# Performance work log

Measured on AMD Instinct MI355X. Metric: run time of the kernel, lower is better.

The kernel has to match this reference:

```python
import jax, jax.numpy as jnp
import numpy as np

DIM_MODEL = 512
HEADS = 8
DIM_HEAD = 64
HIDDEN = HEADS * DIM_HEAD
SCALE = DIM_HEAD ** -0.5
GN_EPS = 1e-5


def setup_inputs() -> dict:
    key = jax.random.key(0)
    ks = jax.random.split(key, 7)
    b, t = 8, 4096
    x = jax.random.normal(ks[0], (b, DIM_MODEL, t), dtype=jnp.float32)
    mask = jax.random.randint(ks[1], (b, t), 0, 2) == 1  # bool padding mask
    # 1x1 convs are plain channel matmuls; kernels squeezed to 2D
    w_qkv = jax.random.normal(ks[2], (3 * HIDDEN, DIM_MODEL), dtype=jnp.float32) * (DIM_MODEL ** -0.5)
    w_out = jax.random.normal(ks[3], (DIM_MODEL, HIDDEN), dtype=jnp.float32) * (HIDDEN ** -0.5)
    b_out = jax.random.normal(ks[4], (DIM_MODEL,), dtype=jnp.float32) * 0.01
    gn_gamma = jnp.ones((DIM_MODEL,), dtype=jnp.float32)
    gn_beta = jnp.zeros((DIM_MODEL,), dtype=jnp.float32)
    return {"x": x, "mask": mask, "w_qkv": w_qkv, "w_out": w_out,
            "b_out": b_out, "gn_gamma": gn_gamma, "gn_beta": gn_beta}


def reference(x, mask, w_qkv, w_out, b_out, gn_gamma, gn_beta):
    b, c, t = x.shape
    # to_qkv: 1x1 conv == channel matmul -> [b, 3*hidden, t]
    qkv = jnp.einsum('oc,bct->bot', w_qkv, x)
    q, k, v = jnp.split(qkv, 3, axis=1)
    # 'b (h d) t -> b h d t'
    q = q.reshape(b, HEADS, DIM_HEAD, t)
    k = k.reshape(b, HEADS, DIM_HEAD, t)
    v = v.reshape(b, HEADS, DIM_HEAD, t)
    # additive mask: 0.0 where True, 1e-12 where False; broadcast 'b t -> b 1 1 t'
    maskf = jnp.where(mask, 0.0, 1e-12)[:, None, None, :].astype(x.dtype)
    q = jax.nn.softmax(q, axis=-2) * SCALE            # softmax over feature dim d
    k = jax.nn.softmax(k + maskf, axis=-1)            # softmax over time dim t
    # linear attention: O(t * d * e)
    context = jnp.einsum('bhdn,bhen->bhde', k, v)      # [b, h, d, e]
    out = jnp.einsum('bhde,bhdn->bhen', context, q)    # [b, h, e, t]
    out = out.reshape(b, HIDDEN, t)                    # 'b h e t -> b (h e) t'
    # to_out: 1x1 conv with bias, then GroupNorm(1, dim_model)
    y = jnp.einsum('oc,bct->bot', w_out, out) + b_out[None, :, None]
    mu = jnp.mean(y, axis=(1, 2), keepdims=True)
    var = jnp.var(y, axis=(1, 2), keepdims=True)
    y = (y - mu) * jax.lax.rsqrt(var + GN_EPS)
    return y * gn_gamma[None, :, None] + gn_beta[None, :, None]
```

## Files before the change

### kernel.cpp

```cpp
#include <hip/hip_runtime.h>
#include <stdint.h>

typedef unsigned short u16;
using f32x4 = __attribute__((ext_vector_type(4))) float;
using s16x8 = __attribute__((ext_vector_type(8))) short;

#define MFMA_BF16(a, b, c) __builtin_amdgcn_mfma_f32_16x16x32_bf16((a), (b), (c), 0, 0, 0)

#define GLOAD_LDS16(gptr, lptr)                                                               \
  __builtin_amdgcn_global_load_lds((const __attribute__((address_space(1))) uint32_t*)(gptr), \
                                   (__attribute__((address_space(3))) uint32_t*)(lptr), 16, 0, 0)

__device__ __forceinline__ u16 f2bf(float f) {
  union { float f; uint32_t u; } v; v.f = f;
  uint32_t r = v.u + 0x7fffu + ((v.u >> 16) & 1u);
  return (u16)(r >> 16);
}
__device__ __forceinline__ float bf2f(u16 h) {
  union { uint32_t u; float f; } v; v.u = ((uint32_t)h) << 16;
  return v.f;
}

__global__ void k_transpose_x(const float* __restrict__ x, u16* __restrict__ xT,
                              const float* __restrict__ wq, const float* __restrict__ wo,
                              u16* __restrict__ wqb, u16* __restrict__ wob) {
  if (blockIdx.z == 8) {
    const int nq = 1536 * 512 / 4;
    const int no = 512 * 512 / 4;
    int bid = blockIdx.y * 64 + blockIdx.x;
#pragma unroll
    for (int rep = 0; rep < 2; ++rep) {
      int i = bid * 256 + threadIdx.x + rep * 131072;
      if (i < nq) {
        float4 v = ((const float4*)wq)[i];
        u16* o = wqb + i * 4;
        o[0] = f2bf(v.x); o[1] = f2bf(v.y); o[2] = f2bf(v.z); o[3] = f2bf(v.w);
      } else if (i < nq + no) {
        int j = i - nq;
        float4 v = ((const float4*)wo)[j];
        u16* o = wob + j * 4;
        o[0] = f2bf(v.x); o[1] = f2bf(v.y); o[2] = f2bf(v.z); o[3] = f2bf(v.w);
      }
    }
    return;
  }
  __shared__ u16 tile[64][68];
  int b = blockIdx.z, c0 = blockIdx.y * 64, t0 = blockIdx.x * 64;
  const float* xp = x + ((size_t)b * 512 + c0) * 4096 + t0;
#pragma unroll
  for (int it = 0; it < 4; ++it) {
    int r = it * 16 + (threadIdx.x >> 4), c4 = (threadIdx.x & 15) * 4;
    float4 v = *(const float4*)(xp + (size_t)r * 4096 + c4);
    tile[r][c4 + 0] = f2bf(v.x);
    tile[r][c4 + 1] = f2bf(v.y);
    tile[r][c4 + 2] = f2bf(v.z);
    tile[r][c4 + 3] = f2bf(v.w);
  }
  __syncthreads();
  u16* op = xT + ((size_t)b * 4096 + t0) * 512 + c0;
#pragma unroll
  for (int it = 0; it < 2; ++it) {
    int tr = it * 32 + (threadIdx.x >> 3), cb = (threadIdx.x & 7) * 8;
    s16x8 o;
#pragma unroll
    for (int jj = 0; jj < 8; ++jj) o[jj] = tile[cb + jj][tr];
    *(s16x8*)(op + (size_t)tr * 512 + cb) = o;
  }
}

__launch_bounds__(256, 2)
__global__ void k_gemm_qkv(const u16* __restrict__ A, const u16* __restrict__ BT,
                           u16* __restrict__ C, u16* __restrict__ qT,
                           float* __restrict__ spart) {
  __shared__ s16x8 As8[1024];
  __shared__ s16x8 Bs8[1024];
  __shared__ float ksums[4][64];
  int b = blockIdx.z;
  int m0 = blockIdx.y * 128, n0 = blockIdx.x * 128;
  const u16* Ab = A + (size_t)m0 * 512;
  const u16* Bb = BT + ((size_t)b * 4096 + n0) * 512;
  int tid = threadIdx.x, w = tid >> 6, lane = tid & 63;
  int wm = (w >> 1) * 64, wn = (w & 1) * 64;
  f32x4 acc[4][4] = {};
  for (int kt = 0; kt < 8; ++kt) {
    if (kt) __syncthreads();
#pragma unroll
    for (int it = 0; it < 4; ++it) {
      int L = (w * 4 + it) * 64 + lane;
      int r = L >> 3;
      int lc = (L & 7) ^ (r & 7);
      GLOAD_LDS16(Ab + (size_t)r * 512 + kt * 64 + lc * 8, ((char*)As8) + (w * 4 + it) * 1024);
      GLOAD_LDS16(Bb + (size_t)r * 512 + kt * 64 + lc * 8, ((char*)Bs8) + (w * 4 + it) * 1024);
    }
    asm volatile("s_waitcnt vmcnt(0)");
    __syncthreads();
#pragma unroll
    for (int kk = 0; kk < 2; ++kk) {
      int cb = kk * 4 + (lane >> 4);
      s16x8 af[4], bfr[4];
#pragma unroll
      for (int mi = 0; mi < 4; ++mi) {
        int r = wm + mi * 16 + (lane & 15);
        af[mi] = As8[r * 8 + (cb ^ (r & 7))];
      }
#pragma unroll
      for (int ni = 0; ni < 4; ++ni) {
        int r = wn + ni * 16 + (lane & 15);
        bfr[ni] = Bs8[r * 8 + (cb ^ (r & 7))];
      }
#pragma unroll
      for (int mi = 0; mi < 4; ++mi)
#pragma unroll
        for (int ni = 0; ni < 4; ++ni)
          acc[mi][ni] = MFMA_BF16(af[mi], bfr[ni], acc[mi][ni]);
    }
  }
  if (blockIdx.y < 4) {
    int head = (m0 >> 6) + (wm >> 6);
    int bh = b * 8 + head;
#pragma unroll
    for (int ni = 0; ni < 4; ++ni) {
      float mx = -1e30f;
#pragma unroll
      for (int mi = 0; mi < 4; ++mi)
#pragma unroll
        for (int j = 0; j < 4; ++j) mx = fmaxf(mx, acc[mi][ni][j]);
      mx = fmaxf(mx, __shfl_xor(mx, 16));
      mx = fmaxf(mx, __shfl_xor(mx, 32));
      float e[4][4];
      float s = 0.f;
#pragma unroll
      for (int mi = 0; mi < 4; ++mi)
#pragma unroll
        for (int j = 0; j < 4; ++j) { e[mi][j] = __expf(acc[mi][ni][j] - mx); s += e[mi][j]; }
      s += __shfl_xor(s, 16);
      s += __shfl_xor(s, 32);
      float sc = 0.125f / s;
      int t = n0 + wn + ni * 16 + (lane & 15);
      u16* op = qT + ((size_t)bh * 4096 + t) * 64 + (lane >> 4) * 4;
#pragma unroll
      for (int mi = 0; mi < 4; ++mi) {
        union { u16 u[4]; uint2 v; } pk;
#pragma unroll
        for (int j = 0; j < 4; ++j) pk.u[j] = f2bf(e[mi][j] * sc);
        *(uint2*)(op + mi * 16) = pk.v;
      }
    }
  } else if (blockIdx.y < 8) {
    u16* Cb = C + ((size_t)b * 1536 + m0) * 4096 + n0;
#pragma unroll
    for (int mi = 0; mi < 4; ++mi)
#pragma unroll
      for (int j = 0; j < 4; ++j) {
        int mm = wm + mi * 16 + (lane >> 4) * 4 + j;
        float t = 0.f;
#pragma unroll
        for (int ni = 0; ni < 4; ++ni) {
          int nn = wn + ni * 16 + (lane & 15);
          float e = __expf(acc[mi][ni][j]);
          t += e;
          Cb[(size_t)mm * 4096 + nn] = f2bf(e);
        }
        t += __shfl_xor(t, 1);
        t += __shfl_xor(t, 2);
        t += __shfl_xor(t, 4);
        t += __shfl_xor(t, 8);
        if ((lane & 15) == 0) ksums[w][mi * 16 + (lane >> 4) * 4 + j] = t;
      }
    __syncthreads();
    if (tid < 128) {
      int hr = tid >> 6, r = tid & 63;
      float v = ksums[hr * 2][r] + ksums[hr * 2 + 1][r];
      spart[((size_t)b * 512 + (m0 - 512) + hr * 64 + r) * 32 + blockIdx.x] = v;
    }
  } else {
    u16* Cb = C + ((size_t)b * 1536 + m0) * 4096 + n0;
#pragma unroll
    for (int mi = 0; mi < 4; ++mi)
#pragma unroll
      for (int ni = 0; ni < 4; ++ni)
#pragma unroll
        for (int j = 0; j < 4; ++j) {
          int mm = wm + mi * 16 + (lane >> 4) * 4 + j;
          int nn = wn + ni * 16 + (lane & 15);
          Cb[(size_t)mm * 4096 + nn] = f2bf(acc[mi][ni][j]);
        }
  }
}

__global__ void k_context_part(const u16* __restrict__ qkv, float* __restrict__ ctxp) {
  int s = blockIdx.x, bh = blockIdx.y;
  int b = bh >> 3, h = bh & 7;
  int w = threadIdx.x >> 6, lane = threadIdx.x & 63;
  int hi = lane >> 4, lo = lane & 15;
  const u16* vb = qkv + ((size_t)b * 1536 + 1024 + h * 64) * 4096 + s * 256;
  const u16* kb = qkv + ((size_t)b * 1536 + 512 + h * 64) * 4096 + s * 256;
  int d = w * 16 + lo;
  f32x4 acc[4] = {};
#pragma unroll
  for (int st = 0; st < 8; ++st) {
    int nn = st * 32 + hi * 8;
    s16x8 bexp = *(const s16x8*)(kb + (size_t)d * 4096 + nn);
#pragma unroll
    for (int ei = 0; ei < 4; ++ei) {
      s16x8 a = *(const s16x8*)(vb + (size_t)(ei * 16 + lo) * 4096 + nn);
      acc[ei] = MFMA_BF16(a, bexp, acc[ei]);
    }
  }
  float* cp = ctxp + ((size_t)bh * 16 + s) * 4096;
#pragma unroll
  for (int ei = 0; ei < 4; ++ei) {
    float4 o;
    o.x = acc[ei][0]; o.y = acc[ei][1]; o.z = acc[ei][2]; o.w = acc[ei][3];
    *(float4*)&cp[(size_t)d * 64 + ei * 16 + hi * 4] = o;
  }
}

__global__ void k_ctx_reduce(const float* __restrict__ ctxp, const float* __restrict__ spart,
                             u16* __restrict__ Bg) {
  int q = blockIdx.x, bh = blockIdx.y;
  int b = bh >> 3, h = bh & 7;
  __shared__ float sinv[4];
  int tid = threadIdx.x;
  if (tid < 4) {
    int hd = h * 64 + q * 4 + tid;
    const float* sp = spart + ((size_t)b * 512 + hd) * 32;
    float s = 0.f;
#pragma unroll
    for (int xx = 0; xx < 32; ++xx) s += sp[xx];
    sinv[tid] = 1.f / s;
  }
  __syncthreads();
  int pos = q * 256 + tid;
  float v = 0.f;
#pragma unroll
  for (int si = 0; si < 16; ++si) v += ctxp[((size_t)bh * 16 + si) * 4096 + pos];
  Bg[(size_t)bh * 4096 + pos] = f2bf(v * sinv[(pos >> 6) & 3]);
}

__global__ void k_wfused(const u16* __restrict__ wout, const u16* __restrict__ Bg,
                         u16* __restrict__ Wf) {
  int bh = blockIdx.x;
  int b = bh >> 3, h = bh & 7;
  int w = threadIdx.x >> 6, lane = threadIdx.x & 63;
  int hi = lane >> 4, lo = lane & 15;
  const u16* Bb = Bg + (size_t)bh * 4096;
  const u16* Ab = wout + (size_t)h * 64;
  f32x4 acc[8][4] = {};
#pragma unroll
  for (int ks = 0; ks < 2; ++ks) {
    s16x8 bfr[4];
#pragma unroll
    for (int ni = 0; ni < 4; ++ni)
      bfr[ni] = *(const s16x8*)(Bb + (size_t)(ni * 16 + lo) * 64 + ks * 32 + hi * 8);
#pragma unroll
    for (int mi = 0; mi < 8; ++mi) {
      s16x8 a = *(const s16x8*)(Ab + (size_t)(w * 128 + mi * 16 + lo) * 512 + ks * 32 + hi * 8);
#pragma unroll
      for (int ni = 0; ni < 4; ++ni) acc[mi][ni] = MFMA_BF16(a, bfr[ni], acc[mi][ni]);
    }
  }
#pragma unroll
  for (int mi = 0; mi < 8; ++mi)
#pragma unroll
    for (int ni = 0; ni < 4; ++ni) {
      int m = w * 128 + mi * 16 + hi * 4;
      int d = ni * 16 + lo;
#pragma unroll
      for (int j = 0; j < 4; ++j)
        Wf[((size_t)b * 512 + m + j) * 512 + h * 64 + d] = f2bf(acc[mi][ni][j]);
    }
}

__launch_bounds__(256, 2)
__global__ void k_gemm_final(const u16* __restrict__ Wf, const u16* __restrict__ qT,
                             u16* __restrict__ Ybf, const float* __restrict__ bias,
                             float2* __restrict__ part2) {
  __shared__ s16x8 As8[1024];
  __shared__ s16x8 Bs8[1024];
  int b = blockIdx.z;
  int m0 = blockIdx.y * 128, n0 = blockIdx.x * 128;
  const u16* Ab = Wf + ((size_t)b * 512 + m0) * 512;
  const u16* qTb = qT + (size_t)b * 8 * 4096 * 64;
  int tid = threadIdx.x, w = tid >> 6, lane = tid & 63;
  int wm = (w >> 1) * 64, wn = (w & 1) * 64;
  f32x4 acc[4][4] = {};
  for (int kt = 0; kt < 8; ++kt) {
    if (kt) __syncthreads();
#pragma unroll
    for (int it = 0; it < 4; ++it) {
      int L = (w * 4 + it) * 64 + lane;
      int r = L >> 3;
      int lc = (L & 7) ^ (r & 7);
      GLOAD_LDS16(Ab + (size_t)r * 512 + kt * 64 + lc * 8, ((char*)As8) + (w * 4 + it) * 1024);
      int G = kt * 8 + lc;
      GLOAD_LDS16(qTb + ((size_t)(G >> 3) * 4096 + n0 + r) * 64 + (G & 7) * 8,
                  ((char*)Bs8) + (w * 4 + it) * 1024);
    }
    asm volatile("s_waitcnt vmcnt(0)");
    __syncthreads();
#pragma unroll
    for (int kk = 0; kk < 2; ++kk) {
      int cb = kk * 4 + (lane >> 4);
      s16x8 af[4], bfr[4];
#pragma unroll
      for (int mi = 0; mi < 4; ++mi) {
        int r = wm + mi * 16 + (lane & 15);
        af[mi] = As8[r * 8 + (cb ^ (r & 7))];
      }
#pragma unroll
      for (int ni = 0; ni < 4; ++ni) {
        int r = wn + ni * 16 + (lane & 15);
        bfr[ni] = Bs8[r * 8 + (cb ^ (r & 7))];
      }
#pragma unroll
      for (int mi = 0; mi < 4; ++mi)
#pragma unroll
        for (int ni = 0; ni < 4; ++ni)
          acc[mi][ni] = MFMA_BF16(af[mi], bfr[ni], acc[mi][ni]);
    }
  }
  u16* Yb = Ybf + ((size_t)b * 512 + m0) * 4096 + n0;
  float sm = 0.f, ssm = 0.f;
#pragma unroll
  for (int mi = 0; mi < 4; ++mi)
#pragma unroll
    for (int j = 0; j < 4; ++j) {
      int mm = wm + mi * 16 + (lane >> 4) * 4 + j;
      float bo = bias[m0 + mm];
#pragma unroll
      for (int ni = 0; ni < 4; ++ni) {
        int nn = wn + ni * 16 + (lane & 15);
        float vv = acc[mi][ni][j] + bo;
        sm += vv;
        ssm += vv * vv;
        Yb[(size_t)mm * 4096 + nn] = f2bf(vv);
      }
    }
#pragma unroll
  for (int off = 32; off; off >>= 1) { sm += __shfl_xor(sm, off); ssm += __shfl_xor(ssm, off); }
  __shared__ float sr[4], ssr[4];
  if (lane == 0) { sr[w] = sm; ssr[w] = ssm; }
  __syncthreads();
  if (tid == 0) {
    float2 o;
    o.x = sr[0] + sr[1] + sr[2] + sr[3];
    o.y = ssr[0] + ssr[1] + ssr[2] + ssr[3];
    part2[((size_t)b * 4 + blockIdx.y) * 32 + blockIdx.x] = o;
  }
}

__global__ void k_gn_norm(const u16* __restrict__ ybf, float* __restrict__ y,
                          const float2* __restrict__ part2,
                          const float* __restrict__ gamma, const float* __restrict__ beta) {
  int b = blockIdx.y;
  float s = 0.f, ss = 0.f;
#pragma unroll 8
  for (int i = 0; i < 128; ++i) { float2 pp = part2[b * 128 + i]; s += pp.x; ss += pp.y; }
  const float N = 512.f * 4096.f;
  float mu = s / N;
  float var = ss / N - mu * mu;
  float rstd = rsqrtf(var + 1e-5f);
  size_t base = ((size_t)b << 21) + (size_t)blockIdx.x * 16384;
  const s16x8* ip = (const s16x8*)(ybf + base);
  float4* opf = (float4*)(y + base);
#pragma unroll
  for (int i = 0; i < 8; ++i) {
    int idx = threadIdx.x + i * 256;
    int loc = (int)(blockIdx.x * 16384) + idx * 8;
    int c = loc >> 12;
    float g = gamma[c] * rstd, bt = beta[c];
    s16x8 v = ip[idx];
    float4 o0, o1;
    o0.x = (bf2f((u16)v[0]) - mu) * g + bt;
    o0.y = (bf2f((u16)v[1]) - mu) * g + bt;
    o0.z = (bf2f((u16)v[2]) - mu) * g + bt;
    o0.w = (bf2f((u16)v[3]) - mu) * g + bt;
    o1.x = (bf2f((u16)v[4]) - mu) * g + bt;
    o1.y = (bf2f((u16)v[5]) - mu) * g + bt;
    o1.z = (bf2f((u16)v[6]) - mu) * g + bt;
    o1.w = (bf2f((u16)v[7]) - mu) * g + bt;
    opf[idx * 2] = o0;
    opf[idx * 2 + 1] = o1;
  }
}

extern "C" void kernel_launch(void* const* d_in, const int* in_sizes, int n_in,
                              void* d_out, int out_size, void* d_ws, size_t ws_size,
                              hipStream_t stream) {
  const float* x     = (const float*)d_in[0];
  const float* wqkv  = (const float*)d_in[2];
  const float* wout  = (const float*)d_in[3];
  const float* bout  = (const float*)d_in[4];
  const float* gamma = (const float*)d_in[5];
  const float* beta  = (const float*)d_in[6];
  float* y = (float*)d_out;

  char* ws = (char*)d_ws;
  u16*    qkv_b = (u16*)ws;
  u16*    ybf   = (u16*)ws;
  u16*    xT    = (u16*)(ws + 100663296);
  float*  ctxp  = (float*)(ws + 100663296);
  u16*    Bg    = (u16*)(ws + 117702656);
  u16*    qT    = (u16*)(ws + 134217728);
  u16*    wqkvb = (u16*)(ws + 167772160);
  u16*    woutb = (u16*)(ws + 169345024);
  u16*    Wfused= (u16*)(ws + 169869312);
  float2* part2 = (float2*)(ws + 174063616);
  float*  spart = (float*)(ws + 174071808);

  {
    dim3 g(64, 8, 9);
    k_transpose_x<<<g, 256, 0, stream>>>(x, xT, wqkv, wout, wqkvb, woutb);
  }
  {
    dim3 g(32, 12, 8);
    k_gemm_qkv<<<g, 256, 0, stream>>>(wqkvb, xT, qkv_b, qT, spart);
  }
  {
    dim3 g(16, 64);
    k_context_part<<<g, 256, 0, stream>>>(qkv_b, ctxp);
  }
  {
    dim3 g(16, 64);
    k_ctx_reduce<<<g, 256, 0, stream>>>(ctxp, spart, Bg);
  }
  k_wfused<<<64, 256, 0, stream>>>(woutb, Bg, Wfused);
  {
    dim3 g(32, 4, 8);
    k_gemm_final<<<g, 256, 0, stream>>>(Wfused, qT, ybf, bout, part2);
  }
  {
    dim3 g(128, 8);
    k_gn_norm<<<g, 256, 0, stream>>>(ybf, y, part2, gamma, beta);
  }
}
```

Baseline: 174.8 us.

## Compute context via exp(K)·Xᵀ then multiply by W_v, skipping V materialization

The V projection is no longer computed or stored. The code forms G = exp(K)·Xᵀ per batch, a 512x512 product over time split into two halves, then multiplies by W_v inside a fused kernel that also applies the softmax normalisation and builds the fused output weight. This removes the V GEMM and its 32MB bf16 write and read, and merges the context partial and reduce kernels. In exchange it adds a bf16 copy of x, a larger K-dim GEMM (512x512x4096 per batch), and extra bf16 rounding of G.

After: 203.6 us. 16.5% more time.

```diff
diff --git a/kernel.cpp b/kernel.cpp
--- a/kernel.cpp
+++ b/kernel.cpp
@@ -22,6 +22,7 @@
 }
 
 __global__ void k_transpose_x(const float* __restrict__ x, u16* __restrict__ xT,
+                              u16* __restrict__ xbf,
                               const float* __restrict__ wq, const float* __restrict__ wo,
                               u16* __restrict__ wqb, u16* __restrict__ wob) {
   if (blockIdx.z == 8) {
@@ -51,10 +52,13 @@
   for (int it = 0; it < 4; ++it) {
     int r = it * 16 + (threadIdx.x >> 4), c4 = (threadIdx.x & 15) * 4;
     float4 v = *(const float4*)(xp + (size_t)r * 4096 + c4);
-    tile[r][c4 + 0] = f2bf(v.x);
-    tile[r][c4 + 1] = f2bf(v.y);
-    tile[r][c4 + 2] = f2bf(v.z);
-    tile[r][c4 + 3] = f2bf(v.w);
+    union { u16 u[4]; uint2 q; } pk;
+    pk.u[0] = f2bf(v.x); pk.u[1] = f2bf(v.y); pk.u[2] = f2bf(v.z); pk.u[3] = f2bf(v.w);
+    tile[r][c4 + 0] = pk.u[0];
+    tile[r][c4 + 1] = pk.u[1];
+    tile[r][c4 + 2] = pk.u[2];
+    tile[r][c4 + 3] = pk.u[3];
+    *(uint2*)(xbf + ((size_t)b * 512 + c0 + r) * 4096 + t0 + c4) = pk.q;
   }
   __syncthreads();
   u16* op = xT + ((size_t)b * 4096 + t0) * 512 + c0;
@@ -70,7 +74,7 @@
 
 __launch_bounds__(256, 2)
 __global__ void k_gemm_qkv(const u16* __restrict__ A, const u16* __restrict__ BT,
-                           u16* __restrict__ C, u16* __restrict__ qT,
+                           u16* __restrict__ ek, u16* __restrict__ qT,
                            float* __restrict__ spart) {
   __shared__ s16x8 As8[1024];
   __shared__ s16x8 Bs8[1024];
@@ -146,8 +150,8 @@
         *(uint2*)(op + mi * 16) = pk.v;
       }
     }
-  } else if (blockIdx.y < 8) {
-    u16* Cb = C + ((size_t)b * 1536 + m0) * 4096 + n0;
+  } else {
+    u16* Cb = ek + ((size_t)b * 512 + (m0 - 512)) * 4096 + n0;
 #pragma unroll
     for (int mi = 0; mi < 4; ++mi)
 #pragma unroll
@@ -173,78 +177,108 @@
       float v = ksums[hr * 2][r] + ksums[hr * 2 + 1][r];
       spart[((size_t)b * 512 + (m0 - 512) + hr * 64 + r) * 32 + blockIdx.x] = v;
     }
-  } else {
-    u16* Cb = C + ((size_t)b * 1536 + m0) * 4096 + n0;
-#pragma unroll
-    for (int mi = 0; mi < 4; ++mi)
-#pragma unroll
-      for (int ni = 0; ni < 4; ++ni)
-#pragma unroll
-        for (int j = 0; j < 4; ++j) {
-          int mm = wm + mi * 16 + (lane >> 4) * 4 + j;
-          int nn = wn + ni * 16 + (lane & 15);
-          Cb[(size_t)mm * 4096 + nn] = f2bf(acc[mi][ni][j]);
-        }
-  }
-}
-
-__global__ void k_context_part(const u16* __restrict__ qkv, float* __restrict__ ctxp) {
-  int s = blockIdx.x, bh = blockIdx.y;
+  }
+}
+
+__launch_bounds__(256, 2)
+__global__ void k_gemm_G(const u16* __restrict__ ek, const u16* __restrict__ xbf,
+                         u16* __restrict__ Gt) {
+  __shared__ s16x8 As8[1024];
+  __shared__ s16x8 Bs8[1024];
+  int z = blockIdx.z;
+  int b = z >> 1, half = z & 1;
+  int m0 = blockIdx.y * 128, n0 = blockIdx.x * 128;
+  const u16* Ab = ek + ((size_t)b * 512 + m0) * 4096 + half * 2048;
+  const u16* Bb = xbf + ((size_t)b * 512 + n0) * 4096 + half * 2048;
+  int tid = threadIdx.x, w = tid >> 6, lane = tid & 63;
+  int wm = (w >> 1) * 64, wn = (w & 1) * 64;
+  f32x4 acc[4][4] = {};
+  for (int kt = 0; kt < 32; ++kt) {
+    if (kt) __syncthreads();
+#pragma unroll
+    for (int it = 0; it < 4; ++it) {
+      int L = (w * 4 + it) * 64 + lane;
+      int r = L >> 3;
+      int lc = (L & 7) ^ (r & 7);
+      GLOAD_LDS16(Ab + (size_t)r * 4096 + kt * 64 + lc * 8, ((char*)As8) + (w * 4 + it) * 1024);
+      GLOAD_LDS16(Bb + (size_t)r * 4096 + kt * 64 + lc * 8, ((char*)Bs8) + (w * 4 + it) * 1024);
+    }
+    asm volatile("s_waitcnt vmcnt(0)");
+    __syncthreads();
+#pragma unroll
+    for (int kk = 0; kk < 2; ++kk) {
+      int cb = kk * 4 + (lane >> 4);
+      s16x8 af[4], bfr[4];
+#pragma unroll
+      for (int mi = 0; mi < 4; ++mi) {
+        int r = wm + mi * 16 + (lane & 15);
+        af[mi] = As8[r * 8 + (cb ^ (r & 7))];
+      }
+#pragma unroll
+      for (int ni = 0; ni < 4; ++ni) {
+        int r = wn + ni * 16 + (lane & 15);
+        bfr[ni] = Bs8[r * 8 + (cb ^ (r & 7))];
+      }
+#pragma unroll
+      for (int mi = 0; mi < 4; ++mi)
+#pragma unroll
+        for (int ni = 0; ni < 4; ++ni)
+          acc[mi][ni] = MFMA_BF16(af[mi], bfr[ni], acc[mi][ni]);
+    }
+  }
+  u16* Cb = Gt + (((size_t)half * 8 + b) * 512 + m0) * 512 + n0;
+#pragma unroll
+  for (int mi = 0; mi < 4; ++mi)
+#pragma unroll
+    for (int ni = 0; ni < 4; ++ni)
+#pragma unroll
+      for (int j = 0; j < 4; ++j) {
+        int mm = wm + mi * 16 + (lane >> 4) * 4 + j;
+        int nn = wn + ni * 16 + (lane & 15);
+        Cb[(size_t)mm * 512 + nn] = f2bf(acc[mi][ni][j]);
+      }
+}
+
+__global__ void k_ctx_wfused(const u16* __restrict__ Gt, const float* __restrict__ spart,
+                             const u16* __restrict__ wqkvb, const u16* __restrict__ wout,
+                             u16* __restrict__ Wf) {
+  __shared__ float sinv[64];
+  __shared__ __align__(16) u16 Bgl[64 * 72];
+  int bh = blockIdx.x;
   int b = bh >> 3, h = bh & 7;
-  int w = threadIdx.x >> 6, lane = threadIdx.x & 63;
-  int hi = lane >> 4, lo = lane & 15;
-  const u16* vb = qkv + ((size_t)b * 1536 + 1024 + h * 64) * 4096 + s * 256;
-  const u16* kb = qkv + ((size_t)b * 1536 + 512 + h * 64) * 4096 + s * 256;
-  int d = w * 16 + lo;
-  f32x4 acc[4] = {};
-#pragma unroll
-  for (int st = 0; st < 8; ++st) {
-    int nn = st * 32 + hi * 8;
-    s16x8 bexp = *(const s16x8*)(kb + (size_t)d * 4096 + nn);
-#pragma unroll
-    for (int ei = 0; ei < 4; ++ei) {
-      s16x8 a = *(const s16x8*)(vb + (size_t)(ei * 16 + lo) * 4096 + nn);
-      acc[ei] = MFMA_BF16(a, bexp, acc[ei]);
-    }
-  }
-  float* cp = ctxp + ((size_t)bh * 16 + s) * 4096;
-#pragma unroll
-  for (int ei = 0; ei < 4; ++ei) {
-    float4 o;
-    o.x = acc[ei][0]; o.y = acc[ei][1]; o.z = acc[ei][2]; o.w = acc[ei][3];
-    *(float4*)&cp[(size_t)d * 64 + ei * 16 + hi * 4] = o;
-  }
-}
-
-__global__ void k_ctx_reduce(const float* __restrict__ ctxp, const float* __restrict__ spart,
-                             u16* __restrict__ Bg) {
-  int q = blockIdx.x, bh = blockIdx.y;
-  int b = bh >> 3, h = bh & 7;
-  __shared__ float sinv[4];
   int tid = threadIdx.x;
-  if (tid < 4) {
-    int hd = h * 64 + q * 4 + tid;
-    const float* sp = spart + ((size_t)b * 512 + hd) * 32;
+  if (tid < 64) {
+    const float* sp = spart + ((size_t)b * 512 + h * 64 + tid) * 32;
     float s = 0.f;
 #pragma unroll
     for (int xx = 0; xx < 32; ++xx) s += sp[xx];
     sinv[tid] = 1.f / s;
   }
   __syncthreads();
-  int pos = q * 256 + tid;
-  float v = 0.f;
-#pragma unroll
-  for (int si = 0; si < 16; ++si) v += ctxp[((size_t)bh * 16 + si) * 4096 + pos];
-  Bg[(size_t)bh * 4096 + pos] = f2bf(v * sinv[(pos >> 6) & 3]);
-}
-
-__global__ void k_wfused(const u16* __restrict__ wout, const u16* __restrict__ Bg,
-                         u16* __restrict__ Wf) {
-  int bh = blockIdx.x;
-  int b = bh >> 3, h = bh & 7;
-  int w = threadIdx.x >> 6, lane = threadIdx.x & 63;
-  int hi = lane >> 4, lo = lane & 15;
-  const u16* Bb = Bg + (size_t)bh * 4096;
+  int w = tid >> 6, lane = tid & 63, hi = lane >> 4, lo = lane & 15;
+  const u16* Wv = wqkvb + (size_t)(1024 + h * 64) * 512;
+  f32x4 cacc[4] = {};
+#pragma unroll
+  for (int half = 0; half < 2; ++half) {
+    const u16* Ga = Gt + (((size_t)half * 8 + b) * 512 + h * 64 + w * 16 + lo) * 512;
+#pragma unroll
+    for (int ks = 0; ks < 16; ++ks) {
+      s16x8 ga = *(const s16x8*)(Ga + ks * 32 + hi * 8);
+#pragma unroll
+      for (int ni = 0; ni < 4; ++ni) {
+        s16x8 wv = *(const s16x8*)(Wv + (size_t)(ni * 16 + lo) * 512 + ks * 32 + hi * 8);
+        cacc[ni] = MFMA_BF16(ga, wv, cacc[ni]);
+      }
+    }
+  }
+#pragma unroll
+  for (int ni = 0; ni < 4; ++ni)
+#pragma unroll
+    for (int j = 0; j < 4; ++j) {
+      int d = w * 16 + hi * 4 + j;
+      Bgl[d * 72 + ni * 16 + lo] = f2bf(cacc[ni][j] * sinv[d]);
+    }
+  __syncthreads();
   const u16* Ab = wout + (size_t)h * 64;
   f32x4 acc[8][4] = {};
 #pragma unroll
@@ -252,7 +286,7 @@
     s16x8 bfr[4];
 #pragma unroll
     for (int ni = 0; ni < 4; ++ni)
-      bfr[ni] = *(const s16x8*)(Bb + (size_t)(ni * 16 + lo) * 64 + ks * 32 + hi * 8);
+      bfr[ni] = *(const s16x8*)&Bgl[(ni * 16 + lo) * 72 + ks * 32 + hi * 8];
 #pragma unroll
     for (int mi = 0; mi < 8; ++mi) {
       s16x8 a = *(const s16x8*)(Ab + (size_t)(w * 128 + mi * 16 + lo) * 512 + ks * 32 + hi * 8);
@@ -397,35 +431,31 @@
   float* y = (float*)d_out;
 
   char* ws = (char*)d_ws;
-  u16*    qkv_b = (u16*)ws;
-  u16*    ybf   = (u16*)ws;
-  u16*    xT    = (u16*)(ws + 100663296);
-  float*  ctxp  = (float*)(ws + 100663296);
-  u16*    Bg    = (u16*)(ws + 117702656);
-  u16*    qT    = (u16*)(ws + 134217728);
-  u16*    wqkvb = (u16*)(ws + 167772160);
-  u16*    woutb = (u16*)(ws + 169345024);
-  u16*    Wfused= (u16*)(ws + 169869312);
-  float2* part2 = (float2*)(ws + 174063616);
-  float*  spart = (float*)(ws + 174071808);
+  u16*    ek    = (u16*)ws;
+  u16*    xT    = (u16*)(ws + 33554432);
+  u16*    xbf   = (u16*)(ws + 67108864);
+  u16*    ybf   = xbf;
+  u16*    qT    = (u16*)(ws + 100663296);
+  u16*    Gt    = (u16*)(ws + 134217728);
+  u16*    wqkvb = (u16*)(ws + 142606336);
+  u16*    woutb = (u16*)(ws + 144179200);
+  u16*    Wfused= (u16*)(ws + 144703488);
+  float*  spart = (float*)(ws + 148897792);
+  float2* part2 = (float2*)(ws + 149422080);
 
   {
     dim3 g(64, 8, 9);
-    k_transpose_x<<<g, 256, 0, stream>>>(x, xT, wqkv, wout, wqkvb, woutb);
+    k_transpose_x<<<g, 256, 0, stream>>>(x, xT, xbf, wqkv, wout, wqkvb, woutb);
   }
   {
-    dim3 g(32, 12, 8);
-    k_gemm_qkv<<<g, 256, 0, stream>>>(wqkvb, xT, qkv_b, qT, spart);
+    dim3 g(32, 8, 8);
+    k_gemm_qkv<<<g, 256, 0, stream>>>(wqkvb, xT, ek, qT, spart);
   }
   {
-    dim3 g(16, 64);
-    k_context_part<<<g, 256, 0, stream>>>(qkv_b, ctxp);
-  }
-  {
-    dim3 g(16, 64);
-    k_ctx_reduce<<<g, 256, 0, stream>>>(ctxp, spart, Bg);
-  }
-  k_wfused<<<64, 256, 0, stream>>>(woutb, Bg, Wfused);
+    dim3 g(4, 4, 16);
+    k_gemm_G<<<g, 256, 0, stream>>>(ek, xbf, Gt);
+  }
+  k_ctx_wfused<<<64, 256, 0, stream>>>(Gt, spart, wqkvb, woutb, Wfused);
   {
     dim3 g(32, 4, 8);
     k_gemm_final<<<g, 256, 0, stream>>>(Wfused, qT, ybf, bout, part2);
```

## Use 256x256 double-buffered 8-wave GEMM tiles for QKV and output projections

Applied to the files above, without the earlier changes.

Both bf16 GEMMs are rebuilt on a shared core macro with 256x256 block tiles, 512 threads (8 waves of 128x64), and double-buffered LDS. The next k-tile's global-to-LDS loads are interleaved between MFMA groups, and s_setprio raises priority around the MFMA bursts. The aim is more data reuse per LDS load and overlap of memory traffic with matrix math. The cost is 132KB of dynamic LDS per block and far fewer blocks (768 and 256), so occupancy and wave-quantization tail effects on the GPU become a risk; partial-sum buffers and their reducers are resized to match.

New measurement: 167.6 us, median of 3. 4.1% less time.

```diff
diff --git a/kernel.cpp b/kernel.cpp
--- a/kernel.cpp
+++ b/kernel.cpp
@@ -68,125 +68,251 @@
   }
 }
 
-__launch_bounds__(256, 2)
+#define STAGE_A16(u, ktile, bf)                                                        \
+  { int L = (u)*512 + tid; int r = L >> 3, pc = L & 7; int lc = pc ^ (r & 7);          \
+    GLOAD_LDS16(Ab + (size_t)r * 512 + (ktile) * 64 + lc * 8,                          \
+                ((char*)AL) + (bf) * 32768 + (size_t)L * 16); }
+#define STAGE_B16(u, ktile, bf)                                                        \
+  { int L = (u)*512 + tid; int r = L >> 3, pc = L & 7; int lc = pc ^ (r & 7);          \
+    GLOAD_LDS16(BSRCX(r, ktile, lc),                                                   \
+                ((char*)BL) + (bf) * 32768 + (size_t)L * 16); }
+
+#define GEMM256_CORE()                                                                 \
+  s16x8* AL = (s16x8*)lds;                                                             \
+  s16x8* BL = (s16x8*)(lds + 65536);                                                   \
+  int tid = threadIdx.x, w = tid >> 6, lane = tid & 63;                                \
+  int wr = w >> 2, wc = w & 3;                                                         \
+  int hi = lane >> 4, lo = lane & 15;                                                  \
+  f32x4 acc[8][4] = {};                                                                \
+  _Pragma("unroll")                                                                    \
+  for (int u = 0; u < 4; ++u) STAGE_A16(u, 0, 0);                                      \
+  _Pragma("unroll")                                                                    \
+  for (int u = 0; u < 4; ++u) STAGE_B16(u, 0, 0);                                      \
+  asm volatile("s_waitcnt vmcnt(0)" ::: "memory");                                     \
+  __syncthreads();                                                                     \
+  int cur = 0;                                                                         \
+  _Pragma("unroll 2")                                                                  \
+  for (int kt = 0; kt < 8; ++kt) {                                                     \
+    const s16x8* Ac = AL + cur * 2048;                                                 \
+    const s16x8* Bc = BL + cur * 2048;                                                 \
+    int nxt = cur ^ 1;                                                                 \
+    bool pf = (kt < 7);                                                                \
+    s16x8 af[4][2], b0[2][2], b1[2][2];                                                \
+    _Pragma("unroll")                                                                  \
+    for (int mi = 0; mi < 4; ++mi) {                                                   \
+      int r = wr * 128 + mi * 16 + lo;                                                 \
+      _Pragma("unroll")                                                                \
+      for (int kk = 0; kk < 2; ++kk) {                                                 \
+        int lc = kk * 4 + hi;                                                          \
+        af[mi][kk] = Ac[r * 8 + (lc ^ (r & 7))];                                       \
+      }                                                                                \
+    }                                                                                  \
+    _Pragma("unroll")                                                                  \
+    for (int ni = 0; ni < 2; ++ni) {                                                   \
+      int r = wc * 64 + ni * 16 + lo;                                                  \
+      _Pragma("unroll")                                                                \
+      for (int kk = 0; kk < 2; ++kk) {                                                 \
+        int lc = kk * 4 + hi;                                                          \
+        b0[ni][kk] = Bc[r * 8 + (lc ^ (r & 7))];                                       \
+      }                                                                                \
+    }                                                                                  \
+    if (pf) { STAGE_A16(0, kt + 1, nxt); STAGE_A16(1, kt + 1, nxt); }                  \
+    __builtin_amdgcn_s_setprio(1);                                                     \
+    _Pragma("unroll")                                                                  \
+    for (int mi = 0; mi < 4; ++mi)                                                     \
+      _Pragma("unroll")                                                                \
+      for (int ni = 0; ni < 2; ++ni)                                                   \
+        _Pragma("unroll")                                                              \
+        for (int kk = 0; kk < 2; ++kk)                                                 \
+          acc[mi][ni] = MFMA_BF16(af[mi][kk], b0[ni][kk], acc[mi][ni]);                \
+    __builtin_amdgcn_s_setprio(0);                                                     \
+    _Pragma("unroll")                                                                  \
+    for (int ni = 0; ni < 2; ++ni) {                                                   \
+      int r = wc * 64 + (ni + 2) * 16 + lo;                                            \
+      _Pragma("unroll")                                                                \
+      for (int kk = 0; kk < 2; ++kk) {                                                 \
+        int lc = kk * 4 + hi;                                                          \
+        b1[ni][kk] = Bc[r * 8 + (lc ^ (r & 7))];                                       \
+      }                                                                                \
+    }                                                                                  \
+    if (pf) { STAGE_A16(2, kt + 1, nxt); STAGE_A16(3, kt + 1, nxt); }                  \
+    __builtin_amdgcn_s_setprio(1);                                                     \
+    _Pragma("unroll")                                                                  \
+    for (int mi = 0; mi < 4; ++mi)                                                     \
+      _Pragma("unroll")                                                                \
+      for (int ni = 0; ni < 2; ++ni)                                                   \
+        _Pragma("unroll")                                                              \
+        for (int kk = 0; kk < 2; ++kk)                                                 \
+          acc[mi][ni + 2] = MFMA_BF16(af[mi][kk], b1[ni][kk], acc[mi][ni + 2]);        \
+    __builtin_amdgcn_s_setprio(0);                                                     \
+    _Pragma("unroll")                                                                  \
+    for (int mi = 0; mi < 4; ++mi) {                                                   \
+      int r = wr * 128 + 64 + mi * 16 + lo;                                            \
+      _Pragma("unroll")                                                                \
+      for (int kk = 0; kk < 2; ++kk) {                                                 \
+        int lc = kk * 4 + hi;                                                          \
+        af[mi][kk] = Ac[r * 8 + (lc ^ (r & 7))];                                       \
+      }                                                                                \
+    }                                                                                  \
+    if (pf) { STAGE_B16(0, kt + 1, nxt); STAGE_B16(1, kt + 1, nxt); }                  \
+    __builtin_amdgcn_s_setprio(1);                                                     \
+    _Pragma("unroll")                                                                  \
+    for (int mi = 0; mi < 4; ++mi)                                                     \
+      _Pragma("unroll")                                                                \
+      for (int ni = 0; ni < 2; ++ni)                                                   \
+        _Pragma("unroll")                                                              \
+        for (int kk = 0; kk < 2; ++kk)                                                 \
+          acc[mi + 4][ni + 2] = MFMA_BF16(af[mi][kk], b1[ni][kk], acc[mi + 4][ni + 2]);\
+    __builtin_amdgcn_s_setprio(0);                                                     \
+    if (pf) { STAGE_B16(2, kt + 1, nxt); STAGE_B16(3, kt + 1, nxt); }                  \
+    __builtin_amdgcn_s_setprio(1);                                                     \
+    _Pragma("unroll")                                                                  \
+    for (int mi = 0; mi < 4; ++mi)                                                     \
+      _Pragma("unroll")                                                                \
+      for (int ni = 0; ni < 2; ++ni)                                                   \
+        _Pragma("unroll")                                                              \
+        for (int kk = 0; kk < 2; ++kk)                                                 \
+          acc[mi + 4][ni] = MFMA_BF16(af[mi][kk], b0[ni][kk], acc[mi + 4][ni]);        \
+    __builtin_amdgcn_s_setprio(0);                                                     \
+    asm volatile("s_waitcnt vmcnt(0)" ::: "memory");                                   \
+    __syncthreads();                                                                   \
+    cur = nxt;                                                                         \
+  }
+
+#define BSRCX(r, ktile, lc) (Bb + (size_t)(r) * 512 + (ktile) * 64 + (lc) * 8)
+__launch_bounds__(512, 2)
 __global__ void k_gemm_qkv(const u16* __restrict__ A, const u16* __restrict__ BT,
                            u16* __restrict__ C, u16* __restrict__ qT,
                            float* __restrict__ spart) {
-  __shared__ s16x8 As8[1024];
-  __shared__ s16x8 Bs8[1024];
-  __shared__ float ksums[4][64];
+  extern __shared__ char lds[];
   int b = blockIdx.z;
-  int m0 = blockIdx.y * 128, n0 = blockIdx.x * 128;
+  int m0 = blockIdx.y * 256, n0 = blockIdx.x * 256;
   const u16* Ab = A + (size_t)m0 * 512;
   const u16* Bb = BT + ((size_t)b * 4096 + n0) * 512;
-  int tid = threadIdx.x, w = tid >> 6, lane = tid & 63;
-  int wm = (w >> 1) * 64, wn = (w & 1) * 64;
-  f32x4 acc[4][4] = {};
-  for (int kt = 0; kt < 8; ++kt) {
-    if (kt) __syncthreads();
-#pragma unroll
-    for (int it = 0; it < 4; ++it) {
-      int L = (w * 4 + it) * 64 + lane;
-      int r = L >> 3;
-      int lc = (L & 7) ^ (r & 7);
-      GLOAD_LDS16(Ab + (size_t)r * 512 + kt * 64 + lc * 8, ((char*)As8) + (w * 4 + it) * 1024);
-      GLOAD_LDS16(Bb + (size_t)r * 512 + kt * 64 + lc * 8, ((char*)Bs8) + (w * 4 + it) * 1024);
-    }
-    asm volatile("s_waitcnt vmcnt(0)");
-    __syncthreads();
-#pragma unroll
-    for (int kk = 0; kk < 2; ++kk) {
-      int cb = kk * 4 + (lane >> 4);
-      s16x8 af[4], bfr[4];
-#pragma unroll
-      for (int mi = 0; mi < 4; ++mi) {
-        int r = wm + mi * 16 + (lane & 15);
-        af[mi] = As8[r * 8 + (cb ^ (r & 7))];
+  GEMM256_CORE()
+  if (blockIdx.y < 2) {
+#pragma unroll
+    for (int hb = 0; hb < 2; ++hb) {
+      int head = (int)blockIdx.y * 4 + wr * 2 + hb;
+      int bh = b * 8 + head;
+#pragma unroll
+      for (int ni = 0; ni < 4; ++ni) {
+        float mx = -1e30f;
+#pragma unroll
+        for (int mi = 0; mi < 4; ++mi)
+#pragma unroll
+          for (int j = 0; j < 4; ++j) mx = fmaxf(mx, acc[hb * 4 + mi][ni][j]);
+        mx = fmaxf(mx, __shfl_xor(mx, 16));
+        mx = fmaxf(mx, __shfl_xor(mx, 32));
+        float e[4][4];
+        float s = 0.f;
+#pragma unroll
+        for (int mi = 0; mi < 4; ++mi)
+#pragma unroll
+          for (int j = 0; j < 4; ++j) {
+            e[mi][j] = __expf(acc[hb * 4 + mi][ni][j] - mx);
+            s += e[mi][j];
+          }
+        s += __shfl_xor(s, 16);
+        s += __shfl_xor(s, 32);
+        float sc = 0.125f / s;
+        int t = n0 + wc * 64 + ni * 16 + lo;
+        u16* op = qT + ((size_t)bh * 4096 + t) * 64 + hi * 4;
+#pragma unroll
+        for (int mi = 0; mi < 4; ++mi) {
+          union { u16 u[4]; uint2 v; } pk;
+#pragma unroll
+          for (int j = 0; j < 4; ++j) pk.u[j] = f2bf(e[mi][j] * sc);
+          *(uint2*)(op + mi * 16) = pk.v;
+        }
       }
-#pragma unroll
-      for (int ni = 0; ni < 4; ++ni) {
-        int r = wn + ni * 16 + (lane & 15);
-        bfr[ni] = Bs8[r * 8 + (cb ^ (r & 7))];
-      }
-#pragma unroll
-      for (int mi = 0; mi < 4; ++mi)
-#pragma unroll
-        for (int ni = 0; ni < 4; ++ni)
-          acc[mi][ni] = MFMA_BF16(af[mi], bfr[ni], acc[mi][ni]);
-    }
-  }
-  if (blockIdx.y < 4) {
-    int head = (m0 >> 6) + (wm >> 6);
-    int bh = b * 8 + head;
-#pragma unroll
-    for (int ni = 0; ni < 4; ++ni) {
-      float mx = -1e30f;
-#pragma unroll
-      for (int mi = 0; mi < 4; ++mi)
-#pragma unroll
-        for (int j = 0; j < 4; ++j) mx = fmaxf(mx, acc[mi][ni][j]);
-      mx = fmaxf(mx, __shfl_xor(mx, 16));
-      mx = fmaxf(mx, __shfl_xor(mx, 32));
-      float e[4][4];
-      float s = 0.f;
-#pragma unroll
-      for (int mi = 0; mi < 4; ++mi)
-#pragma unroll
-        for (int j = 0; j < 4; ++j) { e[mi][j] = __expf(acc[mi][ni][j] - mx); s += e[mi][j]; }
-      s += __shfl_xor(s, 16);
-      s += __shfl_xor(s, 32);
-      float sc = 0.125f / s;
-      int t = n0 + wn + ni * 16 + (lane & 15);
-      u16* op = qT + ((size_t)bh * 4096 + t) * 64 + (lane >> 4) * 4;
-#pragma unroll
-      for (int mi = 0; mi < 4; ++mi) {
-        union { u16 u[4]; uint2 v; } pk;
-#pragma unroll
-        for (int j = 0; j < 4; ++j) pk.u[j] = f2bf(e[mi][j] * sc);
-        *(uint2*)(op + mi * 16) = pk.v;
-      }
-    }
-  } else if (blockIdx.y < 8) {
+    }
+  } else if (blockIdx.y < 4) {
     u16* Cb = C + ((size_t)b * 1536 + m0) * 4096 + n0;
-#pragma unroll
-    for (int mi = 0; mi < 4; ++mi)
+    float* ks = (float*)(lds + 131072);
+#pragma unroll
+    for (int mi = 0; mi < 8; ++mi)
 #pragma unroll
       for (int j = 0; j < 4; ++j) {
-        int mm = wm + mi * 16 + (lane >> 4) * 4 + j;
+        int mr = wr * 128 + mi * 16 + hi * 4 + j;
         float t = 0.f;
 #pragma unroll
         for (int ni = 0; ni < 4; ++ni) {
-          int nn = wn + ni * 16 + (lane & 15);
+          int nn = wc * 64 + ni * 16 + lo;
           float e = __expf(acc[mi][ni][j]);
           t += e;
-          Cb[(size_t)mm * 4096 + nn] = f2bf(e);
+          Cb[(size_t)mr * 4096 + nn] = f2bf(e);
         }
         t += __shfl_xor(t, 1);
         t += __shfl_xor(t, 2);
         t += __shfl_xor(t, 4);
         t += __shfl_xor(t, 8);
-        if ((lane & 15) == 0) ksums[w][mi * 16 + (lane >> 4) * 4 + j] = t;
+        if (lo == 0) ks[wc * 256 + mr] = t;
       }
     __syncthreads();
-    if (tid < 128) {
-      int hr = tid >> 6, r = tid & 63;
-      float v = ksums[hr * 2][r] + ksums[hr * 2 + 1][r];
-      spart[((size_t)b * 512 + (m0 - 512) + hr * 64 + r) * 32 + blockIdx.x] = v;
+    if (tid < 256) {
+      float v = ks[tid] + ks[256 + tid] + ks[512 + tid] + ks[768 + tid];
+      spart[((size_t)b * 512 + (m0 - 512) + tid) * 16 + blockIdx.x] = v;
     }
   } else {
     u16* Cb = C + ((size_t)b * 1536 + m0) * 4096 + n0;
 #pragma unroll
-    for (int mi = 0; mi < 4; ++mi)
+    for (int mi = 0; mi < 8; ++mi)
 #pragma unroll
       for (int ni = 0; ni < 4; ++ni)
 #pragma unroll
         for (int j = 0; j < 4; ++j) {
-          int mm = wm + mi * 16 + (lane >> 4) * 4 + j;
-          int nn = wn + ni * 16 + (lane & 15);
-          Cb[(size_t)mm * 4096 + nn] = f2bf(acc[mi][ni][j]);
+          int mr = wr * 128 + mi * 16 + hi * 4 + j;
+          int nn = wc * 64 + ni * 16 + lo;
+          Cb[(size_t)mr * 4096 + nn] = f2bf(acc[mi][ni][j]);
         }
   }
 }
+#undef BSRCX
+
+#define BSRCX(r, ktile, lc) \
+  (qTb + ((size_t)(((ktile) * 8 + (lc)) >> 3) * 4096 + n0 + (r)) * 64 + (((ktile) * 8 + (lc)) & 7) * 8)
+__launch_bounds__(512, 2)
+__global__ void k_gemm_final(const u16* __restrict__ Wf, const u16* __restrict__ qT,
+                             u16* __restrict__ Ybf, const float* __restrict__ bias,
+                             float2* __restrict__ part2) {
+  extern __shared__ char lds[];
+  int b = blockIdx.z;
+  int m0 = blockIdx.y * 256, n0 = blockIdx.x * 256;
+  const u16* Ab = Wf + ((size_t)b * 512 + m0) * 512;
+  const u16* qTb = qT + (size_t)b * 8 * 4096 * 64;
+  GEMM256_CORE()
+  u16* Yb = Ybf + ((size_t)b * 512 + m0) * 4096 + n0;
+  float sm = 0.f, ssm = 0.f;
+#pragma unroll
+  for (int mi = 0; mi < 8; ++mi)
+#pragma unroll
+    for (int j = 0; j < 4; ++j) {
+      int mr = wr * 128 + mi * 16 + hi * 4 + j;
+      float bo = bias[m0 + mr];
+#pragma unroll
+      for (int ni = 0; ni < 4; ++ni) {
+        int nn = wc * 64 + ni * 16 + lo;
+        float vv = acc[mi][ni][j] + bo;
+        sm += vv;
+        ssm += vv * vv;
+        Yb[(size_t)mr * 4096 + nn] = f2bf(vv);
+      }
+    }
+#pragma unroll
+  for (int off = 32; off; off >>= 1) { sm += __shfl_xor(sm, off); ssm += __shfl_xor(ssm, off); }
+  float* sr = (float*)lds;
+  if (lane == 0) { sr[w] = sm; sr[8 + w] = ssm; }
+  __syncthreads();
+  if (tid == 0) {
+    float2 o;
+    o.x = 0.f; o.y = 0.f;
+#pragma unroll
+    for (int i = 0; i < 8; ++i) { o.x += sr[i]; o.y += sr[8 + i]; }
+    part2[((size_t)b * 2 + blockIdx.y) * 16 + blockIdx.x] = o;
+  }
+}
+#undef BSRCX
 
 __global__ void k_context_part(const u16* __restrict__ qkv, float* __restrict__ ctxp) {
   int s = blockIdx.x, bh = blockIdx.y;
@@ -224,10 +350,10 @@
   int tid = threadIdx.x;
   if (tid < 4) {
     int hd = h * 64 + q * 4 + tid;
-    const float* sp = spart + ((size_t)b * 512 + hd) * 32;
+    const float* sp = spart + ((size_t)b * 512 + hd) * 16;
     float s = 0.f;
 #pragma unroll
-    for (int xx = 0; xx < 32; ++xx) s += sp[xx];
+    for (int xx = 0; xx < 16; ++xx) s += sp[xx];
     sinv[tid] = 1.f / s;
   }
   __syncthreads();
@@ -272,91 +398,13 @@
     }
 }
 
-__launch_bounds__(256, 2)
-__global__ void k_gemm_final(const u16* __restrict__ Wf, const u16* __restrict__ qT,
-                             u16* __restrict__ Ybf, const float* __restrict__ bias,
-                             float2* __restrict__ part2) {
-  __shared__ s16x8 As8[1024];
-  __shared__ s16x8 Bs8[1024];
-  int b = blockIdx.z;
-  int m0 = blockIdx.y * 128, n0 = blockIdx.x * 128;
-  const u16* Ab = Wf + ((size_t)b * 512 + m0) * 512;
-  const u16* qTb = qT + (size_t)b * 8 * 4096 * 64;
-  int tid = threadIdx.x, w = tid >> 6, lane = tid & 63;
-  int wm = (w >> 1) * 64, wn = (w & 1) * 64;
-  f32x4 acc[4][4] = {};
-  for (int kt = 0; kt < 8; ++kt) {
-    if (kt) __syncthreads();
-#pragma unroll
-    for (int it = 0; it < 4; ++it) {
-      int L = (w * 4 + it) * 64 + lane;
-      int r = L >> 3;
-      int lc = (L & 7) ^ (r & 7);
-      GLOAD_LDS16(Ab + (size_t)r * 512 + kt * 64 + lc * 8, ((char*)As8) + (w * 4 + it) * 1024);
-      int G = kt * 8 + lc;
-      GLOAD_LDS16(qTb + ((size_t)(G >> 3) * 4096 + n0 + r) * 64 + (G & 7) * 8,
-                  ((char*)Bs8) + (w * 4 + it) * 1024);
-    }
-    asm volatile("s_waitcnt vmcnt(0)");
-    __syncthreads();
-#pragma unroll
-    for (int kk = 0; kk < 2; ++kk) {
-      int cb = kk * 4 + (lane >> 4);
-      s16x8 af[4], bfr[4];
-#pragma unroll
-      for (int mi = 0; mi < 4; ++mi) {
-        int r = wm + mi * 16 + (lane & 15);
-        af[mi] = As8[r * 8 + (cb ^ (r & 7))];
-      }
-#pragma unroll
-      for (int ni = 0; ni < 4; ++ni) {
-        int r = wn + ni * 16 + (lane & 15);
-        bfr[ni] = Bs8[r * 8 + (cb ^ (r & 7))];
-      }
-#pragma unroll
-      for (int mi = 0; mi < 4; ++mi)
-#pragma unroll
-        for (int ni = 0; ni < 4; ++ni)
-          acc[mi][ni] = MFMA_BF16(af[mi], bfr[ni], acc[mi][ni]);
-    }
-  }
-  u16* Yb = Ybf + ((size_t)b * 512 + m0) * 4096 + n0;
-  float sm = 0.f, ssm = 0.f;
-#pragma unroll
-  for (int mi = 0; mi < 4; ++mi)
-#pragma unroll
-    for (int j = 0; j < 4; ++j) {
-      int mm = wm + mi * 16 + (lane >> 4) * 4 + j;
-      float bo = bias[m0 + mm];
-#pragma unroll
-      for (int ni = 0; ni < 4; ++ni) {
-        int nn = wn + ni * 16 + (lane & 15);
-        float vv = acc[mi][ni][j] + bo;
-        sm += vv;
-        ssm += vv * vv;
-        Yb[(size_t)mm * 4096 + nn] = f2bf(vv);
-      }
-    }
-#pragma unroll
-  for (int off = 32; off; off >>= 1) { sm += __shfl_xor(sm, off); ssm += __shfl_xor(ssm, off); }
-  __shared__ float sr[4], ssr[4];
-  if (lane == 0) { sr[w] = sm; ssr[w] = ssm; }
-  __syncthreads();
-  if (tid == 0) {
-    float2 o;
-    o.x = sr[0] + sr[1] + sr[2] + sr[3];
-    o.y = ssr[0] + ssr[1] + ssr[2] + ssr[3];
-    part2[((size_t)b * 4 + blockIdx.y) * 32 + blockIdx.x] = o;
-  }
-}
-
 __global__ void k_gn_norm(const u16* __restrict__ ybf, float* __restrict__ y,
                           const float2* __restrict__ part2,
                           const float* __restrict__ gamma, const float* __restrict__ beta) {
   int b = blockIdx.y;
   float s = 0.f, ss = 0.f;
-#pragma unroll 8
-  for (int i = 0; i < 128; ++i) { float2 pp = part2[b * 128 + i]; s += pp.x; ss += pp.y; }
+#pragma unroll
+  for (int i = 0; i < 32; ++i) { float2 pp = part2[b * 32 + i]; s += pp.x; ss += pp.y; }
   const float N = 512.f * 4096.f;
   float mu = s / N;
   float var = ss / N - mu * mu;
@@ -409,13 +457,19 @@
   float2* part2 = (float2*)(ws + 174063616);
   float*  spart = (float*)(ws + 174071808);
 
+  const int GEMM_LDS = 135168;
+  (void)hipFuncSetAttribute((const void*)k_gemm_qkv,
+                            hipFuncAttributeMaxDynamicSharedMemorySize, GEMM_LDS);
+  (void)hipFuncSetAttribute((const void*)k_gemm_final,
+                            hipFuncAttributeMaxDynamicSharedMemorySize, GEMM_LDS);
+
   {
     dim3 g(64, 8, 9);
     k_transpose_x<<<g, 256, 0, stream>>>(x, xT, wqkv, wout, wqkvb, woutb);
   }
   {
-    dim3 g(32, 12, 8);
-    k_gemm_qkv<<<g, 256, 0, stream>>>(wqkvb, xT, qkv_b, qT, spart);
+    dim3 g(16, 6, 8);
+    k_gemm_qkv<<<g, 512, GEMM_LDS, stream>>>(wqkvb, xT, qkv_b, qT, spart);
   }
   {
     dim3 g(16, 64);
@@ -427,8 +481,8 @@
   }
   k_wfused<<<64, 256, 0, stream>>>(woutb, Bg, Wfused);
   {
-    dim3 g(32, 4, 8);
-    k_gemm_final<<<g, 256, 0, stream>>>(Wfused, qT, ybf, bout, part2);
+    dim3 g(16, 2, 8);
+    k_gemm_final<<<g, 512, GEMM_LDS, stream>>>(Wfused, qT, ybf, bout, part2);
   }
   {
     dim3 g(128, 8);
```
